# Optimization experiments

Measured on AMD Instinct MI355X. Metric: run time of the kernel, lower is better.

The kernel has to match this reference:

```python
import jax, jax.numpy as jnp
import numpy as np

B, S, D, H = 2, 2048, 1024, 16
DK = D // H


def setup_inputs() -> dict:
    key = jax.random.key(0)
    ks = jax.random.split(key, 11)
    inp = {
        'query': jax.random.normal(ks[0], (B, S, D), jnp.float32),
        'key':   jax.random.normal(ks[1], (B, S, D), jnp.float32),
        'value': jax.random.normal(ks[2], (B, S, D), jnp.float32),
        # causal mask, broadcast over heads like mask.unsqueeze(1)
        'mask': jnp.broadcast_to(jnp.tril(jnp.ones((S, S), jnp.int32)), (B, S, S)),
    }
    s = 1.0 / np.sqrt(D)
    for i, nm in enumerate(['q', 'k', 'v', 'o']):
        inp[f'W{nm}'] = jax.random.normal(ks[3 + i], (D, D), jnp.float32) * s
        inp[f'b{nm}'] = jnp.zeros((D,), jnp.float32)
    return inp


def reference(query, key, value, mask, Wq, bq, Wk, bk, Wv, bv, Wo, bo):
    def proj(x, W, b):
        # [B,S,D] -> [B,H,S,DK]
        y = x @ W.T + b
        return y.reshape(B, S, H, DK).transpose(0, 2, 1, 3)

    q = proj(query, Wq, bq)
    k = proj(key, Wk, bk)
    v = proj(value, Wv, bv)

    scores = jnp.einsum('bhsd,bhtd->bhst', q, k) / np.sqrt(DK)
    scores = jnp.where(mask[:, None, :, :] == 0, -1e9, scores)
    p = jax.nn.softmax(scores, axis=-1)  # dropout in eval mode = identity
    x = jnp.einsum('bhst,bhtd->bhsd', p, v)
    x = x.transpose(0, 2, 1, 3).reshape(B, S, D)
    return x @ Wo.T + bo
```

## Files before the change

kernel.cpp:

```cpp
#include <hip/hip_runtime.h>
#include <stdint.h>

#define BB 2
#define SS 2048
#define DD 1024
#define HH 16
#define DKK 64
#define EE 4194304
#define WEE 1048576
#define QSCALE 0.1803368801f

typedef __attribute__((ext_vector_type(8))) short bf16x8;
typedef __attribute__((ext_vector_type(4))) float f32x4;
typedef __attribute__((ext_vector_type(4))) unsigned short u16x4;

__device__ __forceinline__ unsigned short f2bf(float f) {
    union { float f; unsigned int i; } c; c.f = f;
    unsigned int u = c.i;
    return (unsigned short)((u + 0x7FFFu + ((u >> 16) & 1u)) >> 16);
}
__device__ __forceinline__ float bf2f(unsigned short u) {
    union { float f; unsigned int i; } c; c.i = ((unsigned int)u) << 16; return c.f;
}
__device__ __forceinline__ float load1f(const void* p, int idx, int isbf) {
    return isbf ? bf2f(((const unsigned short*)p)[idx]) : ((const float*)p)[idx];
}

#define GLDS16(gp, lp)                                                              \
    __builtin_amdgcn_global_load_lds(                                               \
        (const __attribute__((address_space(1))) void*)(gp),                        \
        (__attribute__((address_space(3))) void*)(lp), 16, 0, 0)

__global__ void detect_dtype_k(const unsigned short* __restrict__ q,
                               int* __restrict__ flag) {
    const int lane = threadIdx.x;
    unsigned short u = q[lane * 2];
    int ex = (u >> 7) & 0xFF;
    bool bad = (ex != 0) && (ex < 110 || ex > 137);
    unsigned long long m = __ballot(bad);
    if (lane == 0) *flag = (__popcll(m) >= 8) ? 0 : 1;
}

__global__ __launch_bounds__(256)
void convert_k(const float* __restrict__ q, const float* __restrict__ k,
               const float* __restrict__ v,
               const float* __restrict__ wq, const float* __restrict__ wk,
               const float* __restrict__ wv, const float* __restrict__ wo,
               unsigned short* __restrict__ Xc, unsigned short* __restrict__ Wc,
               const int* __restrict__ flagp)
{
    if (*flagp) return;
    const size_t e = ((size_t)blockIdx.x * 256 + threadIdx.x) * 8;
    const float* src; unsigned short* dst; size_t off;
    if (e < (size_t)3 * EE) {
        const int t = (int)(e / EE);
        src = (t == 0) ? q : (t == 1) ? k : v;
        off = e - (size_t)t * EE;
        dst = Xc + (size_t)t * EE;
    } else {
        const size_t we = e - (size_t)3 * EE;
        const int t = (int)(we >> 20);
        src = (t == 0) ? wq : (t == 1) ? wk : (t == 2) ? wv : wo;
        off = we & (WEE - 1);
        dst = Wc + (size_t)t * WEE;
    }
    const float4 a = *(const float4*)(src + off);
    const float4 b = *(const float4*)(src + off + 4);
    bf16x8 o;
    o[0] = (short)f2bf(a.x); o[1] = (short)f2bf(a.y);
    o[2] = (short)f2bf(a.z); o[3] = (short)f2bf(a.w);
    o[4] = (short)f2bf(b.x); o[5] = (short)f2bf(b.y);
    o[6] = (short)f2bf(b.z); o[7] = (short)f2bf(b.w);
    *(bf16x8*)(dst + off) = o;
}

__global__ __launch_bounds__(256)
void gemm_qkv(const void* __restrict__ Xq, const void* __restrict__ Xk,
              const void* __restrict__ Xv,
              const void* __restrict__ Wqp, const void* __restrict__ Wkp,
              const void* __restrict__ Wvp,
              const void* __restrict__ bqp, const void* __restrict__ bkp,
              const void* __restrict__ bvp,
              const unsigned short* __restrict__ Xc,
              const unsigned short* __restrict__ Wc,
              unsigned short* __restrict__ qb, unsigned short* __restrict__ kb,
              unsigned short* __restrict__ vtb, const int* __restrict__ flagp)
{
    const int isbf = *flagp;
    const int z = blockIdx.z;
    const unsigned short* Xg = isbf
        ? (const unsigned short*)((z == 0) ? Xq : (z == 1) ? Xk : Xv)
        : Xc + (size_t)z * EE;
    const unsigned short* Wg = isbf
        ? (const unsigned short*)((z == 0) ? Wqp : (z == 1) ? Wkp : Wvp)
        : Wc + (size_t)z * WEE;
    const void* bias = (z == 0) ? bqp : (z == 1) ? bkp : bvp;

    __shared__ __align__(16) unsigned short As[3][128 * 32];
    __shared__ __align__(16) unsigned short Bs[3][128 * 32];

    const int tid  = threadIdx.x;
    const int lane = tid & 63, w = tid >> 6;
    const int l15  = lane & 15, quad = lane >> 4;
    const int wr = (w >> 1) * 64, wc = (w & 1) * 64;
    const int r0 = blockIdx.x * 128, c0 = blockIdx.y * 128;
    const int srow = tid >> 2;
    const int scol = (((tid & 3) ^ ((tid >> 3) & 3)) << 3);
    const int rdo  = ((quad ^ ((l15 >> 1) & 3)) << 3);

    const unsigned short* xp0 = Xg + (size_t)(r0 + srow) * DD + scol;
    const unsigned short* xp1 = Xg + (size_t)(r0 + 64 + srow) * DD + scol;
    const unsigned short* wp0 = Wg + (size_t)(c0 + srow) * DD + scol;
    const unsigned short* wp1 = Wg + (size_t)(c0 + 64 + srow) * DD + scol;

#define STAGE_G(buf, kk)                                                       \
    do {                                                                       \
        GLDS16(xp0 + (kk), &As[buf][tid * 8]);                                 \
        GLDS16(xp1 + (kk), &As[buf][2048 + tid * 8]);                          \
        GLDS16(wp0 + (kk), &Bs[buf][tid * 8]);                                 \
        GLDS16(wp1 + (kk), &Bs[buf][2048 + tid * 8]);                          \
    } while (0)

#define LOADFRAG_G(buf)                                                        \
    do {                                                                       \
        _Pragma("unroll")                                                      \
        for (int mi = 0; mi < 4; ++mi)                                         \
            af[mi] = *(const bf16x8*)(&As[buf][(wr + mi * 16 + l15) * 32 +     \
                                               rdo]);                          \
        _Pragma("unroll")                                                      \
        for (int ni = 0; ni < 4; ++ni)                                         \
            bfr[ni] = *(const bf16x8*)(&Bs[buf][(wc + ni * 16 + l15) * 32 +    \
                                                rdo]);                         \
    } while (0)

#define MFMA_G()                                                               \
    do {                                                                       \
        __builtin_amdgcn_s_setprio(1);                                         \
        _Pragma("unroll")                                                      \
        for (int mi = 0; mi < 4; ++mi)                                         \
            _Pragma("unroll")                                                  \
            for (int ni = 0; ni < 4; ++ni)                                     \
                acc[mi][ni] = __builtin_amdgcn_mfma_f32_16x16x32_bf16(         \
                    af[mi], bfr[ni], acc[mi][ni], 0, 0, 0);                    \
        __builtin_amdgcn_s_setprio(0);                                         \
    } while (0)

#define PHASE_G(cb, nb, kn)                                                    \
    do {                                                                       \
        asm volatile("s_waitcnt vmcnt(4)" ::: "memory");                       \
        __builtin_amdgcn_s_barrier();                                          \
        __builtin_amdgcn_sched_barrier(0);                                     \
        LOADFRAG_G(cb);                                                        \
        STAGE_G(nb, kn);                                                       \
        __builtin_amdgcn_sched_barrier(0);                                     \
        MFMA_G();                                                              \
    } while (0)

    f32x4 acc[4][4] = {};
    bf16x8 af[4], bfr[4];

    STAGE_G(0, 0);
    STAGE_G(1, 32);
    for (int s = 0; s < 30; s += 3) {
        const int k0 = s * 32;
        PHASE_G(0, 2, k0 + 64);
        PHASE_G(1, 0, k0 + 96);
        PHASE_G(2, 1, k0 + 128);
    }
    asm volatile("s_waitcnt vmcnt(4)" ::: "memory");
    __builtin_amdgcn_s_barrier();
    __builtin_amdgcn_sched_barrier(0);
    LOADFRAG_G(0);
    MFMA_G();
    asm volatile("s_waitcnt vmcnt(0)" ::: "memory");
    __builtin_amdgcn_s_barrier();
    __builtin_amdgcn_sched_barrier(0);
    LOADFRAG_G(1);
    MFMA_G();

#pragma unroll
    for (int mi = 0; mi < 4; ++mi) {
#pragma unroll
        for (int ni = 0; ni < 4; ++ni) {
            const int col = c0 + wc + ni * 16 + l15;
            const float bv = load1f(bias, col, isbf);
            const int h = col >> 6, dk = col & 63;
            const int m0 = r0 + wr + mi * 16 + quad * 4;
            const int bb = m0 >> 11, s0 = m0 & (SS - 1);
            const int bh = bb * HH + h;
            if (z == 0) {
#pragma unroll
                for (int r = 0; r < 4; ++r)
                    qb[((size_t)bh * SS + s0 + r) * DKK + dk] =
                        f2bf((acc[mi][ni][r] + bv) * QSCALE);
            } else if (z == 1) {
#pragma unroll
                for (int r = 0; r < 4; ++r) {
                    const int t = s0 + r;
                    kb[((((size_t)bh * 128 + (t >> 4)) * 8 + (dk >> 3)) * 16 +
                        (t & 15)) * 8 + (dk & 7)] = f2bf(acc[mi][ni][r] + bv);
                }
            } else {
                u16x4 pv;
#pragma unroll
                for (int r = 0; r < 4; ++r) pv[r] = f2bf(acc[mi][ni][r] + bv);
                const int t = s0;
                *(u16x4*)&vtb[((((size_t)bh * 64 + (t >> 5)) * 4 + (dk >> 4)) * 64 +
                               ((t >> 3) & 3) * 16 + (dk & 15)) * 8 + (t & 7)] = pv;
            }
        }
    }
#undef STAGE_G
#undef LOADFRAG_G
#undef MFMA_G
#undef PHASE_G
}

template <bool MASKED>
__device__ __forceinline__ void attn_tile(
    const int t0, const int q0, const int l15, const int quad,
    const unsigned short* __restrict__ Kb, const unsigned short* __restrict__ Vb,
    const bf16x8 (&qf)[2], f32x4 (&Oa)[4], float (&ls)[4],
    unsigned short* __restrict__ Pw)
{
    bf16x8 kf[4][2];
#pragma unroll
    for (int ni = 0; ni < 4; ++ni)
#pragma unroll
        for (int ks = 0; ks < 2; ++ks)
            kf[ni][ks] = *(const bf16x8*)(Kb +
                ((size_t)(((t0 >> 4) + ni) * 8 + ks * 4 + quad) * 16 + l15) * 8);

    f32x4 sc[4] = {};
    __builtin_amdgcn_s_setprio(1);
#pragma unroll
    for (int ks = 0; ks < 2; ++ks)
#pragma unroll
        for (int ni = 0; ni < 4; ++ni)
            sc[ni] = __builtin_amdgcn_mfma_f32_16x16x32_bf16(
                qf[ks], kf[ni][ks], sc[ni], 0, 0, 0);
    __builtin_amdgcn_s_setprio(0);

    bf16x8 vf[4][2];
#pragma unroll
    for (int nd = 0; nd < 4; ++nd)
#pragma unroll
        for (int ks = 0; ks < 2; ++ks)
            vf[nd][ks] = *(const bf16x8*)(Vb +
                ((size_t)(((t0 >> 5) + ks) * 4 + nd) * 64 + quad * 16 + l15) * 8);

#pragma unroll
    for (int ni = 0; ni < 4; ++ni)
#pragma unroll
        for (int r = 0; r < 4; ++r) {
            float s = sc[ni][r];
            if (MASKED && (t0 + ni * 16 + l15 > q0 + quad * 4 + r))
                s = -__builtin_inff();
            const float p = exp2f(s);
            const unsigned int pu = __float_as_uint(p);
            ls[r] += __uint_as_float(pu & 0xFFFF0000u);
            Pw[(quad * 4 + r) * 72 + ni * 16 + l15] = (unsigned short)(pu >> 16);
        }

    bf16x8 pf[2];
#pragma unroll
    for (int ks = 0; ks < 2; ++ks)
        pf[ks] = *(const bf16x8*)(Pw + l15 * 72 + ks * 32 + quad * 8);
    __builtin_amdgcn_s_setprio(1);
#pragma unroll
    for (int ks = 0; ks < 2; ++ks)
#pragma unroll
        for (int nd = 0; nd < 4; ++nd)
            Oa[nd] = __builtin_amdgcn_mfma_f32_16x16x32_bf16(
                pf[ks], vf[nd][ks], Oa[nd], 0, 0, 0);
    __builtin_amdgcn_s_setprio(0);
}

__global__ __launch_bounds__(256)
void attn_mfma(const unsigned short* __restrict__ Qg,
               const unsigned short* __restrict__ Kf,
               const unsigned short* __restrict__ Vf,
               unsigned short* __restrict__ Og)
{
    __shared__ __align__(16) unsigned short Ps[4][16 * 72];
    const int tid  = threadIdx.x;
    const int lane = tid & 63, w = tid >> 6;
    const int l15 = lane & 15, quad = lane >> 4;
    const int bh = blockIdx.x;
    const int qt = (gridDim.y - 1 - blockIdx.y) * 4 + w;
    const int q0 = qt * 16;
    unsigned short* Pw = &Ps[w][0];

    const unsigned short* Qb = Qg + (size_t)bh * SS * DKK;
    const unsigned short* Kb = Kf + (size_t)bh * SS * DKK;
    const unsigned short* Vb = Vf + (size_t)bh * SS * DKK;

    bf16x8 qf[2];
#pragma unroll
    for (int ks = 0; ks < 2; ++ks)
        qf[ks] = *(const bf16x8*)(Qb + (size_t)(q0 + l15) * DKK + ks * 32 + quad * 8);

    f32x4 Oa[4] = {};
    float ls[4] = {};
    const int nfull = q0 >> 6;

    for (int tt = 0; tt < nfull; ++tt)
        attn_tile<false>(tt * 64, q0, l15, quad, Kb, Vb, qf, Oa, ls, Pw);
    attn_tile<true>(nfull * 64, q0, l15, quad, Kb, Vb, qf, Oa, ls, Pw);

    const int bb = bh >> 4, h = bh & (HH - 1);
#pragma unroll
    for (int r = 0; r < 4; ++r) {
        float l = ls[r];
        l += __shfl_xor(l, 1);
        l += __shfl_xor(l, 2);
        l += __shfl_xor(l, 4);
        l += __shfl_xor(l, 8);
        const float inv = 1.0f / l;
        const int s = q0 + quad * 4 + r;
#pragma unroll
        for (int nd = 0; nd < 4; ++nd)
            Og[((size_t)bb * SS + s) * DD + h * 64 + nd * 16 + l15] =
                f2bf(Oa[nd][r] * inv);
    }
}

__global__ __launch_bounds__(256)
void gemm_out(const unsigned short* __restrict__ Xa, const void* __restrict__ W,
              const unsigned short* __restrict__ Wcs,
              const void* __restrict__ bias, void* __restrict__ Y,
              const int* __restrict__ flagp)
{
    const int isbf = *flagp;
    const unsigned short* Wg = isbf ? (const unsigned short*)W : Wcs;

    __shared__ __align__(16) unsigned short As[3][64 * 32];
    __shared__ __align__(16) unsigned short Bs[3][128 * 32];

    const int tid  = threadIdx.x;
    const int lane = tid & 63, w = tid >> 6;
    const int l15  = lane & 15, quad = lane >> 4;
    const int wr = (w >> 1) * 32, wc = (w & 1) * 64;
    const int r0 = blockIdx.x * 64, c0 = blockIdx.y * 128;
    const int srow = tid >> 2;
    const int scol = (((tid & 3) ^ ((tid >> 3) & 3)) << 3);
    const int rdo  = ((quad ^ ((l15 >> 1) & 3)) << 3);

    const unsigned short* xp0 = Xa + (size_t)(r0 + srow) * DD + scol;
    const unsigned short* wp0 = Wg + (size_t)(c0 + srow) * DD + scol;
    const unsigned short* wp1 = Wg + (size_t)(c0 + 64 + srow) * DD + scol;

#define STAGE_O(buf, kk)                                                       \
    do {                                                                       \
        GLDS16(xp0 + (kk), &As[buf][tid * 8]);                                 \
        GLDS16(wp0 + (kk), &Bs[buf][tid * 8]);                                 \
        GLDS16(wp1 + (kk), &Bs[buf][2048 + tid * 8]);                          \
    } while (0)

#define LOADFRAG_O(buf)                                                        \
    do {                                                                       \
        _Pragma("unroll")                                                      \
        for (int mi = 0; mi < 2; ++mi)                                         \
            af[mi] = *(const bf16x8*)(&As[buf][(wr + mi * 16 + l15) * 32 +     \
                                               rdo]);                          \
        _Pragma("unroll")                                                      \
        for (int ni = 0; ni < 4; ++ni)                                         \
            bfr[ni] = *(const bf16x8*)(&Bs[buf][(wc + ni * 16 + l15) * 32 +    \
                                                rdo]);                         \
    } while (0)

#define MFMA_O()                                                               \
    do {                                                                       \
        __builtin_amdgcn_s_setprio(1);                                         \
        _Pragma("unroll")                                                      \
        for (int mi = 0; mi < 2; ++mi)                                         \
            _Pragma("unroll")                                                  \
            for (int ni = 0; ni < 4; ++ni)                                     \
                acc[mi][ni] = __builtin_amdgcn_mfma_f32_16x16x32_bf16(         \
                    af[mi], bfr[ni], acc[mi][ni], 0, 0, 0);                    \
        __builtin_amdgcn_s_setprio(0);                                         \
    } while (0)

#define PHASE_O(cb, nb, kn)                                                    \
    do {                                                                       \
        asm volatile("s_waitcnt vmcnt(3)" ::: "memory");                       \
        __builtin_amdgcn_s_barrier();                                          \
        __builtin_amdgcn_sched_barrier(0);                                     \
        LOADFRAG_O(cb);                                                        \
        STAGE_O(nb, kn);                                                       \
        __builtin_amdgcn_sched_barrier(0);                                     \
        MFMA_O();                                                              \
    } while (0)

    f32x4 acc[2][4] = {};
    bf16x8 af[2], bfr[4];

    STAGE_O(0, 0);
    STAGE_O(1, 32);
    for (int s = 0; s < 30; s += 3) {
        const int k0 = s * 32;
        PHASE_O(0, 2, k0 + 64);
        PHASE_O(1, 0, k0 + 96);
        PHASE_O(2, 1, k0 + 128);
    }
    asm volatile("s_waitcnt vmcnt(3)" ::: "memory");
    __builtin_amdgcn_s_barrier();
    __builtin_amdgcn_sched_barrier(0);
    LOADFRAG_O(0);
    MFMA_O();
    asm volatile("s_waitcnt vmcnt(0)" ::: "memory");
    __builtin_amdgcn_s_barrier();
    __builtin_amdgcn_sched_barrier(0);
    LOADFRAG_O(1);
    MFMA_O();

#pragma unroll
    for (int mi = 0; mi < 2; ++mi) {
#pragma unroll
        for (int ni = 0; ni < 4; ++ni) {
            const int col = c0 + wc + ni * 16 + l15;
            const float bv = load1f(bias, col, isbf);
            const int m0 = r0 + wr + mi * 16 + quad * 4;
#pragma unroll
            for (int r = 0; r < 4; ++r) {
                const float val = acc[mi][ni][r] + bv;
                if (isbf) ((unsigned short*)Y)[(size_t)(m0 + r) * DD + col] = f2bf(val);
                else      ((float*)Y)[(size_t)(m0 + r) * DD + col] = val;
            }
        }
    }
#undef STAGE_O
#undef LOADFRAG_O
#undef MFMA_O
#undef PHASE_O
}

extern "C" void kernel_launch(void* const* d_in, const int* in_sizes, int n_in,
                              void* d_out, int out_size, void* d_ws, size_t ws_size,
                              hipStream_t stream)
{
    const void* query = d_in[0];
    const void* key   = d_in[1];
    const void* value = d_in[2];
    const void* Wq = d_in[4];  const void* bq = d_in[5];
    const void* Wk = d_in[6];  const void* bk = d_in[7];
    const void* Wv = d_in[8];  const void* bv = d_in[9];
    const void* Wo = d_in[10]; const void* bo = d_in[11];

    int* flag = (int*)d_ws;
    unsigned short* base = (unsigned short*)((char*)d_ws + 256);
    const size_t E = EE;
    unsigned short* qb  = base;
    unsigned short* kb  = base + E;
    unsigned short* vtb = base + 2 * E;
    unsigned short* Wc  = base + 3 * E;
    unsigned short* Xc  = base + 4 * E;
    unsigned short* ab  = Xc;

    detect_dtype_k<<<1, 64, 0, stream>>>((const unsigned short*)query, flag);
    convert_k<<<8192, 256, 0, stream>>>((const float*)query, (const float*)key,
                                        (const float*)value, (const float*)Wq,
                                        (const float*)Wk, (const float*)Wv,
                                        (const float*)Wo, Xc, Wc, flag);
    gemm_qkv<<<dim3(32, 8, 3), 256, 0, stream>>>(query, key, value, Wq, Wk, Wv,
                                                 bq, bk, bv, Xc, Wc,
                                                 qb, kb, vtb, flag);
    attn_mfma<<<dim3(32, 32), 256, 0, stream>>>(qb, kb, vtb, ab);
    gemm_out<<<dim3(64, 8), 256, 0, stream>>>(ab, Wo, Wc + 3 * (size_t)WEE, bo,
                                              d_out, flag);
}
```

Before: 233.4 us.

## Split causal key range across wave pairs in attention and combine via LDS

Each block now covers two 16-row query tiles instead of four. Each tile is handled by a pair of waves that split its causal key range: one wave takes the first half of the full tiles, the other takes the rest plus the masked diagonal tile. The second wave writes its unnormalized accumulators and row sums to shared memory, and the first wave adds them, normalizes and stores the result. The grid doubles, which shortens the serial chain per wave and evens out causal imbalance. The cost is an extra block-wide barrier, shared-memory traffic, and more blocks each loading Q.

```diff
diff --git a/kernel.cpp b/kernel.cpp
--- a/kernel.cpp
+++ b/kernel.cpp
@@ -283,11 +283,15 @@
                unsigned short* __restrict__ Og)
 {
     __shared__ __align__(16) unsigned short Ps[4][16 * 72];
+    __shared__ __align__(16) float Cb[2][16][68];
+    __shared__ float Ls[2][16];
     const int tid  = threadIdx.x;
     const int lane = tid & 63, w = tid >> 6;
     const int l15 = lane & 15, quad = lane >> 4;
     const int bh = blockIdx.x;
-    const int qt = (gridDim.y - 1 - blockIdx.y) * 4 + w;
+    const int g = gridDim.y - 1 - blockIdx.y;
+    const int qtl = w >> 1, half = w & 1;
+    const int qt = g * 2 + qtl;
     const int q0 = qt * 16;
     unsigned short* Pw = &Ps[w][0];
 
@@ -302,13 +306,19 @@
 
     f32x4 Oa[4] = {};
     float ls[4] = {};
-    const int nfull = q0 >> 6;
-
-    for (int tt = 0; tt < nfull; ++tt)
-        attn_tile<false>(tt * 64, q0, l15, quad, Kb, Vb, qf, Oa, ls, Pw);
-    attn_tile<true>(nfull * 64, q0, l15, quad, Kb, Vb, qf, Oa, ls, Pw);
-
-    const int bb = bh >> 4, h = bh & (HH - 1);
+    const int NT = (q0 >> 6) + 1;
+    const int hsp = NT >> 1;
+
+    if (half == 0) {
+        for (int t = 0; t < hsp; ++t)
+            attn_tile<false>(t * 64, q0, l15, quad, Kb, Vb, qf, Oa, ls, Pw);
+    } else {
+        for (int t = hsp; t < NT - 1; ++t)
+            attn_tile<false>(t * 64, q0, l15, quad, Kb, Vb, qf, Oa, ls, Pw);
+        attn_tile<true>((NT - 1) * 64, q0, l15, quad, Kb, Vb, qf, Oa, ls, Pw);
+    }
+
+    float lr[4];
 #pragma unroll
     for (int r = 0; r < 4; ++r) {
         float l = ls[r];
@@ -316,12 +326,32 @@
         l += __shfl_xor(l, 2);
         l += __shfl_xor(l, 4);
         l += __shfl_xor(l, 8);
-        const float inv = 1.0f / l;
-        const int s = q0 + quad * 4 + r;
+        lr[r] = l;
+    }
+
+    if (half == 1) {
 #pragma unroll
         for (int nd = 0; nd < 4; ++nd)
-            Og[((size_t)bb * SS + s) * DD + h * 64 + nd * 16 + l15] =
-                f2bf(Oa[nd][r] * inv);
+#pragma unroll
+            for (int r = 0; r < 4; ++r)
+                Cb[qtl][quad * 4 + r][nd * 16 + l15] = Oa[nd][r];
+        if (l15 == 0)
+#pragma unroll
+            for (int r = 0; r < 4; ++r) Ls[qtl][quad * 4 + r] = lr[r];
+    }
+    __syncthreads();
+    if (half == 0) {
+        const int bb = bh >> 4, h = bh & (HH - 1);
+#pragma unroll
+        for (int r = 0; r < 4; ++r) {
+            const int row = quad * 4 + r;
+            const float inv = 1.0f / (lr[r] + Ls[qtl][row]);
+            const int s = q0 + row;
+#pragma unroll
+            for (int nd = 0; nd < 4; ++nd)
+                Og[((size_t)bb * SS + s) * DD + h * 64 + nd * 16 + l15] =
+                    f2bf((Oa[nd][r] + Cb[qtl][row][nd * 16 + l15]) * inv);
+        }
     }
 }
 
@@ -465,7 +495,7 @@
     gemm_qkv<<<dim3(32, 8, 3), 256, 0, stream>>>(query, key, value, Wq, Wk, Wv,
                                                  bq, bk, bv, Xc, Wc,
                                                  qb, kb, vtb, flag);
-    attn_mfma<<<dim3(32, 32), 256, 0, stream>>>(qb, kb, vtb, ab);
+    attn_mfma<<<dim3(32, 64), 256, 0, stream>>>(qb, kb, vtb, ab);
     gemm_out<<<dim3(64, 8), 256, 0, stream>>>(ab, Wo, Wc + 3 * (size_t)WEE, bo,
                                               d_out, flag);
 }
```

Measured after the change: 237.3 us. About the same (+1.7%).
